# Kernel tuning notes

Measured on AMD Instinct MI355X. Metric: run time of the kernel, lower is better.

The kernel has to match this reference:

```python
import jax, jax.numpy as jnp
import numpy as np
from jax import lax

D = 256      # key/query dim
D_F = 256    # diff feature channels
C_TOK = 1    # leading context tokens in query_vit
EPS = 1e-6


def conv2d(x, w, b, pad):
    out = lax.conv_general_dilated(x, w, (1, 1), [(pad, pad), (pad, pad)],
                                   dimension_numbers=('NCHW', 'OIHW', 'NCHW'))
    return out + b[None, :, None, None]


def gn1(x, g, b):
    # GroupNorm with 1 group: normalize over (C,H,W) per sample
    mu = jnp.mean(x, axis=(1, 2, 3), keepdims=True)
    var = jnp.var(x, axis=(1, 2, 3), keepdims=True)
    xn = (x - mu) * lax.rsqrt(var + EPS)
    return xn * g[None, :, None, None] + b[None, :, None, None]


def resize_bilinear_ac(x, Ho, Wo):
    # F.interpolate(mode='bilinear', align_corners=True)
    B, C, H, W = x.shape
    ys = jnp.linspace(0.0, H - 1.0, Ho)
    xs = jnp.linspace(0.0, W - 1.0, Wo)
    y0 = jnp.floor(ys).astype(jnp.int32)
    y1 = jnp.minimum(y0 + 1, H - 1)
    wy = (ys - y0)[None, None, :, None]
    x0 = jnp.floor(xs).astype(jnp.int32)
    x1 = jnp.minimum(x0 + 1, W - 1)
    wx = (xs - x0)[None, None, None, :]
    r = x[:, :, y0, :] * (1.0 - wy) + x[:, :, y1, :] * wy
    return r[:, :, :, x0] * (1.0 - wx) + r[:, :, :, x1] * wx


def setup_inputs() -> dict:
    key = jax.random.key(0)
    ks = jax.random.split(key, 12)
    B, Hd, Wd, Ht, Wt = 8, 64, 64, 32, 32

    def kaiming(k, shape, fan_in):
        return jax.random.normal(k, shape, jnp.float32) * np.sqrt(2.0 / fan_in)

    return {
        'query_vit': jax.random.normal(ks[0], (B, C_TOK + Ht * Wt, D), jnp.float32),
        'feat_diff_cat': jax.random.normal(ks[1], (B, 5 * D_F, Hd, Wd), jnp.float32),
        'rb_w1': kaiming(ks[2], (D_F, 5 * D_F, 3, 3), 5 * D_F * 9), 'rb_b1': jnp.zeros((D_F,), jnp.float32),
        'rb_w2': kaiming(ks[3], (D_F, D_F, 3, 3), D_F * 9), 'rb_b2': jnp.zeros((D_F,), jnp.float32),
        'rb_ws': kaiming(ks[4], (D_F, 5 * D_F, 1, 1), 5 * D_F), 'rb_bs': jnp.zeros((D_F,), jnp.float32),
        'ln_g': jnp.ones((D_F,), jnp.float32), 'ln_b': jnp.zeros((D_F,), jnp.float32),
        'key_w': kaiming(ks[5], (D, D_F, 1, 1), D_F), 'key_b': jnp.zeros((D,), jnp.float32),
        'val_w': kaiming(ks[6], (D_F, D_F, 1, 1), D_F), 'val_b': jnp.zeros((D_F,), jnp.float32),
        'dh0_w': kaiming(ks[7], (D_F, D_F, 3, 3), D_F * 9), 'dh0_b': jnp.zeros((D_F,), jnp.float32),
        'dh1_w': kaiming(ks[8], (D_F, D_F, 3, 3), D_F * 9), 'dh1_b': jnp.zeros((D_F,), jnp.float32),
    }


def reference(query_vit, feat_diff_cat, rb_w1, rb_b1, rb_w2, rb_b2, rb_ws, rb_bs,
              ln_g, ln_b, key_w, key_b, val_w, val_b, dh0_w, dh0_b, dh1_w, dh1_b):
    B, _, h_diff, w_diff = feat_diff_cat.shape
    N = query_vit.shape[1] - C_TOK
    h_trm = w_trm = int(N ** 0.5)

    # ResBlock_ysh(D_f*5 -> D_f): conv3x3 + relu + conv3x3, 1x1-projected residual
    h = jax.nn.relu(conv2d(feat_diff_cat, rb_w1, rb_b1, 1))
    h = conv2d(h, rb_w2, rb_b2, 1)
    feat_diff = jax.nn.relu(h + conv2d(feat_diff_cat, rb_ws, rb_bs, 0))

    fln = gn1(feat_diff, ln_g, ln_b)
    key_diff = conv2d(fln, key_w, key_b, 0).reshape(B, D, -1)          # (B, D, HW)
    value_diff = conv2d(fln, val_w, val_b, 0).reshape(B, D_F, -1)      # (B, Df, HW)
    value_diff = jnp.transpose(value_diff, (0, 2, 1))                  # (B, HW, Df)

    # cross attention: (B, C+N, D) @ (B, D, HW) -> softmax -> @ (B, HW, Df)
    scores = jnp.einsum('bnd,bdm->bnm', query_vit, key_diff) * (D ** -0.5)
    attn = jax.nn.softmax(scores, axis=-1)
    out_cross = jnp.einsum('bnm,bmf->bnf', attn, value_diff)           # (B, C+N, Df)

    out_cross_c = out_cross[:, :C_TOK, :]
    out_p = jnp.transpose(out_cross[:, C_TOK:, :], (0, 2, 1)).reshape(B, D_F, h_trm, w_trm)
    out_p = jax.nn.relu(conv2d(out_p, dh0_w, dh0_b, 1))
    out_p = resize_bilinear_ac(out_p, h_diff, w_diff)
    out_p = out_p + feat_diff                                          # DropPath(0) = identity
    out_p = jax.nn.relu(conv2d(gn1(out_p, ln_g, ln_b), dh1_w, dh1_b, 1)) + out_p
    return out_cross_c, out_p
```

## Files before the change

kernel.cpp:

```cpp
#include <hip/hip_runtime.h>
#include <cstdint>
#include <cstddef>

typedef __attribute__((ext_vector_type(4))) float     f32x4;
typedef __attribute__((ext_vector_type(8))) __bf16    bf16x8;
typedef __attribute__((ext_vector_type(8))) short     short8;
typedef __attribute__((ext_vector_type(4))) unsigned short u16x4;
typedef unsigned short u16;

__device__ __forceinline__ float b2f(u16 u) {
  unsigned x = ((unsigned)u) << 16;
  float f;
  __builtin_memcpy(&f, &x, 4);
  return f;
}
__device__ __forceinline__ u16 f2b(float f) {
  unsigned u;
  __builtin_memcpy(&u, &f, 4);
  return (u16)((u + 0x7FFFu + ((u >> 16) & 1u)) >> 16);
}

struct GP {
  const u16*  A;
  const u16*  B;
  const float* bias;
  const void* aux;
  void*       C;
  float*      out0;
  long long   aBS, bBS, cBS, auxBS;
  int Ktot, Mrows, ldc;
  int cin, logW, wpad, poff;
  float scale;
};

#define GLDS16(g, l)                                                        \
  __builtin_amdgcn_global_load_lds(                                         \
      (const void __attribute__((address_space(1)))*)(g),                   \
      (void __attribute__((address_space(3)))*)(l), 16, 0, 0)

struct G256 {
  const u16* A;
  const u16* B;
  float* P;
  long long aBS;
  int Ktot, cin, logW, wpad, poff;
};

__global__ __launch_bounds__(512, 2) void k_gemm256(G256 gp) {
  const int tid = threadIdx.x;
  const int l = tid & 63, w = tid >> 6;
  const int lr = l & 15, lc = l >> 4;
  const int mt = blockIdx.x, sp = blockIdx.y, b = blockIdx.z;
  const int m0 = mt << 8;
  const int wm = w >> 2, wn = w & 3;

  __shared__ __align__(16) u16 sm[2][32768];
  u16* smb = &sm[0][0];

  f32x4 acc[8][4];
#pragma unroll
  for (int i = 0; i < 8; ++i)
#pragma unroll
    for (int j = 0; j < 4; ++j) acc[i][j] = (f32x4){0.f, 0.f, 0.f, 0.f};

  const u16* Ab = gp.A + (size_t)b * gp.aBS;
  const int slot = l & 3;
  const u16* aS[2];
  const u16* bS[2];
#pragma unroll
  for (int j = 0; j < 2; ++j) {
    const int r = j * 128 + w * 16 + (l >> 2);
    const int p = m0 + r;
    const int y = p >> gp.logW, x = p & ((1 << gp.logW) - 1);
    const int sw = (slot ^ ((r >> 1) & 3)) << 3;
    aS[j] = Ab + (size_t)((y + gp.poff) * gp.wpad + (x + gp.poff)) * gp.cin + sw;
    bS[j] = gp.B + (size_t)r * gp.Ktot + sw;
  }
  auto dstA = [&](int buf, int ks, int j) -> u16* {
    return smb + buf * 32768 + ks * 8192 + (j * 128 + w * 16) * 32 + l * 8;
  };
  auto dstB = [&](int buf, int ks, int j) -> u16* {
    return smb + buf * 32768 + 16384 + ks * 8192 + (j * 128 + w * 16) * 32 + l * 8;
  };

  const int Thalf = (gp.Ktot >> 6) >> 1;
  const int kt0 = sp * Thalf;
  int off = kt0 << 6;
  int tap = off / gp.cin;
  int kcS = off - tap * gp.cin;
  int dxS = tap % 3;
  int tapS = (tap / 3) * gp.wpad + dxS;
  int ktS = kt0;

  auto adv = [&](int& kA, int& kB) {
    kB = ktS << 6;
    kA = tapS * gp.cin + kcS;
    kcS += 64;
    if (kcS == gp.cin) {
      kcS = 0; ++dxS; ++tapS;
      if (dxS == 3) { dxS = 0; tapS += gp.wpad - 3; }
    }
    ++ktS;
  };

  {
    int kA, kB;
    adv(kA, kB);
    GLDS16(aS[0] + kA, dstA(0, 0, 0));
    GLDS16(aS[1] + kA, dstA(0, 0, 1));
    GLDS16(bS[0] + kB, dstB(0, 0, 0));
    GLDS16(bS[1] + kB, dstB(0, 0, 1));
    GLDS16(aS[0] + kA + 32, dstA(0, 1, 0));
    GLDS16(aS[1] + kA + 32, dstA(0, 1, 1));
    GLDS16(bS[0] + kB + 32, dstB(0, 1, 0));
    GLDS16(bS[1] + kB + 32, dstB(0, 1, 1));
  }
  asm volatile("s_waitcnt vmcnt(4)" ::: "memory");
  __builtin_amdgcn_s_barrier();

  const int NT = Thalf;
  for (int t = 0; t < NT; ++t) {
    const int buf = t & 1;
    const char* base = (const char*)smb + buf * 65536;
    const bool pf = (t + 1 < NT);
    int kA = 0, kB = 0;
    if (pf) adv(kA, kB);

    bf16x8 av[4], bv[4];

#pragma unroll
    for (int mi = 0; mi < 4; ++mi) {
      const int row = wm * 128 + mi * 16 + lr;
      av[mi] = *(const bf16x8*)(base + row * 64 + ((lc ^ ((row >> 1) & 3)) << 4));
    }
#pragma unroll
    for (int ni = 0; ni < 4; ++ni) {
      const int row = wn * 64 + ni * 16 + lr;
      bv[ni] = *(const bf16x8*)(base + 32768 + row * 64 +
                                ((lc ^ ((row >> 1) & 3)) << 4));
    }
    if (pf) {
      GLDS16(aS[0] + kA, dstA(buf ^ 1, 0, 0));
      GLDS16(aS[1] + kA, dstA(buf ^ 1, 0, 1));
    }
    __builtin_amdgcn_s_barrier();
    asm volatile("s_waitcnt lgkmcnt(0)" ::: "memory");
    __builtin_amdgcn_sched_barrier(0);
    __builtin_amdgcn_s_setprio(1);
#pragma unroll
    for (int mi = 0; mi < 4; ++mi)
#pragma unroll
      for (int ni = 0; ni < 4; ++ni)
        acc[mi][ni] = __builtin_amdgcn_mfma_f32_16x16x32_bf16(
            av[mi], bv[ni], acc[mi][ni], 0, 0, 0);
    __builtin_amdgcn_s_setprio(0);
    __builtin_amdgcn_sched_barrier(0);
    __builtin_amdgcn_s_barrier();

#pragma unroll
    for (int mi = 0; mi < 4; ++mi) {
      const int row = wm * 128 + (4 + mi) * 16 + lr;
      av[mi] = *(const bf16x8*)(base + row * 64 + ((lc ^ ((row >> 1) & 3)) << 4));
    }
    if (pf) {
      GLDS16(bS[0] + kB, dstB(buf ^ 1, 0, 0));
      GLDS16(bS[1] + kB, dstB(buf ^ 1, 0, 1));
    }
    __builtin_amdgcn_s_barrier();
    asm volatile("s_waitcnt lgkmcnt(0)" ::: "memory");
    __builtin_amdgcn_sched_barrier(0);
    __builtin_amdgcn_s_setprio(1);
#pragma unroll
    for (int mi = 0; mi < 4; ++mi)
#pragma unroll
      for (int ni = 0; ni < 4; ++ni)
        acc[4 + mi][ni] = __builtin_amdgcn_mfma_f32_16x16x32_bf16(
            av[mi], bv[ni], acc[4 + mi][ni], 0, 0, 0);
    __builtin_amdgcn_s_setprio(0);
    __builtin_amdgcn_sched_barrier(0);
    if (pf)
      asm volatile("s_waitcnt vmcnt(4)" ::: "memory");
    else
      asm volatile("s_waitcnt vmcnt(0)" ::: "memory");
    __builtin_amdgcn_s_barrier();

#pragma unroll
    for (int mi = 0; mi < 4; ++mi) {
      const int row = wm * 128 + mi * 16 + lr;
      av[mi] = *(const bf16x8*)(base + 16384 + row * 64 +
                                ((lc ^ ((row >> 1) & 3)) << 4));
    }
#pragma unroll
    for (int ni = 0; ni < 4; ++ni) {
      const int row = wn * 64 + ni * 16 + lr;
      bv[ni] = *(const bf16x8*)(base + 49152 + row * 64 +
                                ((lc ^ ((row >> 1) & 3)) << 4));
    }
    if (pf) {
      GLDS16(aS[0] + kA + 32, dstA(buf ^ 1, 1, 0));
      GLDS16(aS[1] + kA + 32, dstA(buf ^ 1, 1, 1));
    }
    __builtin_amdgcn_s_barrier();
    asm volatile("s_waitcnt lgkmcnt(0)" ::: "memory");
    __builtin_amdgcn_sched_barrier(0);
    __builtin_amdgcn_s_setprio(1);
#pragma unroll
    for (int mi = 0; mi < 4; ++mi)
#pragma unroll
      for (int ni = 0; ni < 4; ++ni)
        acc[mi][ni] = __builtin_amdgcn_mfma_f32_16x16x32_bf16(
            av[mi], bv[ni], acc[mi][ni], 0, 0, 0);
    __builtin_amdgcn_s_setprio(0);
    __builtin_amdgcn_sched_barrier(0);
    __builtin_amdgcn_s_barrier();

#pragma unroll
    for (int mi = 0; mi < 4; ++mi) {
      const int row = wm * 128 + (4 + mi) * 16 + lr;
      av[mi] = *(const bf16x8*)(base + 16384 + row * 64 +
                                ((lc ^ ((row >> 1) & 3)) << 4));
    }
    if (pf) {
      GLDS16(bS[0] + kB + 32, dstB(buf ^ 1, 1, 0));
      GLDS16(bS[1] + kB + 32, dstB(buf ^ 1, 1, 1));
    }
    __builtin_amdgcn_s_barrier();
    asm volatile("s_waitcnt lgkmcnt(0)" ::: "memory");
    __builtin_amdgcn_sched_barrier(0);
    __builtin_amdgcn_s_setprio(1);
#pragma unroll
    for (int mi = 0; mi < 4; ++mi)
#pragma unroll
      for (int ni = 0; ni < 4; ++ni)
        acc[4 + mi][ni] = __builtin_amdgcn_mfma_f32_16x16x32_bf16(
            av[mi], bv[ni], acc[4 + mi][ni], 0, 0, 0);
    __builtin_amdgcn_s_setprio(0);
    __builtin_amdgcn_sched_barrier(0);
    if (pf) {
      asm volatile("s_waitcnt vmcnt(4)" ::: "memory");
      __builtin_amdgcn_s_barrier();
    }
  }

  float* P = gp.P + ((size_t)sp * 128 + b * 16 + mt) * 65536;
#pragma unroll
  for (int mi = 0; mi < 8; ++mi)
#pragma unroll
    for (int ni = 0; ni < 4; ++ni) {
      const int ncol = wn * 64 + ni * 16 + lr;
      const int mloc = wm * 128 + mi * 16 + lc * 4;
#pragma unroll
      for (int r = 0; r < 4; ++r)
        P[(size_t)(mloc + r) * 256 + ncol] = acc[mi][ni][r];
    }
}

__global__ __launch_bounds__(256) void k_reduceH1(const float* __restrict__ P,
                                                  const float* __restrict__ bias,
                                                  u16* __restrict__ o) {
  const int i4 = blockIdx.x * 256 + threadIdx.x;
  const int flat = i4 << 2;
  const int n0 = flat & 255;
  const int mloc = (flat >> 8) & 255;
  const int gm = flat >> 16;
  const f32x4 a = *(const f32x4*)(P + (size_t)gm * 65536 + mloc * 256 + n0);
  const f32x4 c = *(const f32x4*)(P + (size_t)(128 + gm) * 65536 + mloc * 256 + n0);
  const f32x4 bb = *(const f32x4*)(bias + n0);
  const int batch = gm >> 4;
  const int mg = (gm & 15) * 256 + mloc;
  const int y = mg >> 6, x = mg & 63;
  u16x4 r;
#pragma unroll
  for (int k = 0; k < 4; ++k) r[k] = f2b(fmaxf(a[k] + c[k] + bb[k], 0.f));
  *(u16x4*)(o + ((size_t)batch * 4356 + (size_t)(y + 1) * 66 + x + 1) * 256 + n0) = r;
}

template <int AMODE, int CW, bool RELU>
__global__ __launch_bounds__(512, 2) void k_gemm8(GP gp) {
  const int tid = threadIdx.x;
  const int l = tid & 63, w = tid >> 6;
  const int b = blockIdx.z;
  const int m0 = blockIdx.x * 128;
  const int wm = w >> 2, wn = w & 3;

  __shared__ __align__(16) u16 sm[3][24576];

  f32x4 acc[4][4];
#pragma unroll
  for (int i = 0; i < 4; ++i)
#pragma unroll
    for (int j = 0; j < 4; ++j) acc[i][j] = (f32x4){0.f, 0.f, 0.f, 0.f};

  const u16* Ab = gp.A + (size_t)b * gp.aBS;
  const u16* Bb = gp.B + (size_t)b * gp.bBS;
  const int scoff = (((tid & 7) ^ ((tid >> 3) & 7)) << 3);

  const u16* aP[2];
  const u16* bP[4];
#pragma unroll
  for (int i = 0; i < 2; ++i) {
    const int p = m0 + i * 64 + (tid >> 3);
    if (AMODE == 0) {
      const int pc = p < gp.Mrows ? p : gp.Mrows - 1;
      aP[i] = Ab + (size_t)pc * gp.Ktot + scoff;
    } else {
      const int y = p >> gp.logW, x = p & ((1 << gp.logW) - 1);
      aP[i] = Ab + (size_t)((y + gp.poff) * gp.wpad + (x + gp.poff)) * gp.cin +
              scoff;
    }
  }
#pragma unroll
  for (int i = 0; i < 4; ++i)
    bP[i] = Bb + (size_t)(i * 64 + (tid >> 3)) * gp.Ktot + scoff;

  const int NT = gp.Ktot >> 6;
  int kcS = 0, tapS = 0, dxS = 0, ktS = 0;

  auto adv = [&](int& kA, int& kB) {
    kB = ktS << 6;
    if (AMODE == 0) {
      kA = ktS << 6;
    } else {
      kA = tapS * gp.cin + kcS;
      kcS += 64;
      if (kcS == gp.cin) {
        kcS = 0; ++dxS; ++tapS;
        if (dxS == 3) { dxS = 0; tapS += gp.wpad - 3; }
      }
    }
    ++ktS;
  };

#pragma unroll
  for (int pt = 0; pt < 2; ++pt) {
    int kA, kB;
    adv(kA, kB);
    u16* sA = &sm[pt][0] + (w << 9);
    u16* sB = &sm[pt][8192] + (w << 9);
    GLDS16(aP[0] + kA, sA);
    GLDS16(aP[1] + kA, sA + 4096);
    GLDS16(bP[0] + kB, sB);
    GLDS16(bP[1] + kB, sB + 4096);
    GLDS16(bP[2] + kB, sB + 8192);
    GLDS16(bP[3] + kB, sB + 12288);
  }
  asm volatile("s_waitcnt vmcnt(6)" ::: "memory");
  __builtin_amdgcn_s_barrier();

  const int lr = l & 15, lc = l >> 4;
  int bufC = 0, bufS = 2;

  for (int t = 0; t < NT; ++t) {
    const u16* sAc = &sm[bufC][0];
    const u16* sBc = &sm[bufC][8192];
    const bool sOK = (t + 2 < NT);
    int kAs = 0, kBs = 0;
    if (sOK) adv(kAs, kBs);
    u16* sAs = &sm[bufS][0] + (w << 9);
    u16* sBs = &sm[bufS][8192] + (w << 9);

    bf16x8 bv[4][2];
    {
      bf16x8 av[2][2];
#pragma unroll
      for (int mi = 0; mi < 2; ++mi) {
        const int row = wm * 64 + mi * 16 + lr;
#pragma unroll
        for (int ks = 0; ks < 2; ++ks) {
          const int cc = ks * 4 + lc;
          av[mi][ks] =
              *(const bf16x8*)(sAc + row * 64 + ((cc ^ (row & 7)) << 3));
        }
      }
#pragma unroll
      for (int ni = 0; ni < 4; ++ni) {
        const int row = wn * 64 + ni * 16 + lr;
#pragma unroll
        for (int ks = 0; ks < 2; ++ks) {
          const int cc = ks * 4 + lc;
          bv[ni][ks] =
              *(const bf16x8*)(sBc + row * 64 + ((cc ^ (row & 7)) << 3));
        }
      }
      if (sOK) {
        GLDS16(aP[0] + kAs, sAs);
        GLDS16(aP[1] + kAs, sAs + 4096);
        GLDS16(bP[0] + kBs, sBs);
      }
      __builtin_amdgcn_s_barrier();
      asm volatile("s_waitcnt lgkmcnt(0)" ::: "memory");
      __builtin_amdgcn_sched_barrier(0);
      __builtin_amdgcn_s_setprio(1);
#pragma unroll
      for (int ks = 0; ks < 2; ++ks)
#pragma unroll
        for (int mi = 0; mi < 2; ++mi)
#pragma unroll
          for (int ni = 0; ni < 4; ++ni)
            acc[mi][ni] = __builtin_amdgcn_mfma_f32_16x16x32_bf16(
                av[mi][ks], bv[ni][ks], acc[mi][ni], 0, 0, 0);
      __builtin_amdgcn_sched_barrier(0);
      __builtin_amdgcn_s_setprio(0);
    }
    __builtin_amdgcn_s_barrier();
    {
      bf16x8 av[2][2];
#pragma unroll
      for (int mi = 0; mi < 2; ++mi) {
        const int row = wm * 64 + (mi + 2) * 16 + lr;
#pragma unroll
        for (int ks = 0; ks < 2; ++ks) {
          const int cc = ks * 4 + lc;
          av[mi][ks] =
              *(const bf16x8*)(sAc + row * 64 + ((cc ^ (row & 7)) << 3));
        }
      }
      if (sOK) {
        GLDS16(bP[1] + kBs, sBs + 4096);
        GLDS16(bP[2] + kBs, sBs + 8192);
        GLDS16(bP[3] + kBs, sBs + 12288);
      }
      __builtin_amdgcn_s_barrier();
      asm volatile("s_waitcnt lgkmcnt(0)" ::: "memory");
      __builtin_amdgcn_sched_barrier(0);
      __builtin_amdgcn_s_setprio(1);
#pragma unroll
      for (int ks = 0; ks < 2; ++ks)
#pragma unroll
        for (int mi = 0; mi < 2; ++mi)
#pragma unroll
          for (int ni = 0; ni < 4; ++ni)
            acc[mi + 2][ni] = __builtin_amdgcn_mfma_f32_16x16x32_bf16(
                av[mi][ks], bv[ni][ks], acc[mi + 2][ni], 0, 0, 0);
      __builtin_amdgcn_sched_barrier(0);
      __builtin_amdgcn_s_setprio(0);
    }
    if (t + 1 < NT) {
      if (t + 2 < NT)
        asm volatile("s_waitcnt vmcnt(6)" ::: "memory");
      else
        asm volatile("s_waitcnt vmcnt(0)" ::: "memory");
      __builtin_amdgcn_s_barrier();
    }
    bufC = bufC == 2 ? 0 : bufC + 1;
    bufS = bufS == 2 ? 0 : bufS + 1;
  }

#pragma unroll
  for (int mi = 0; mi < 4; ++mi) {
#pragma unroll
    for (int ni = 0; ni < 4; ++ni) {
      const int ncol = wn * 64 + ni * 16 + lr;
      const int mbase = m0 + wm * 64 + mi * 16 + lc * 4;
      const float bv_ = gp.bias ? gp.bias[ncol] : 0.f;
      if constexpr (CW == 0) {
#pragma unroll
        for (int r = 0; r < 4; ++r) {
          float v = acc[mi][ni][r] + bv_;
          if (RELU) v = fmaxf(v, 0.f);
          ((u16*)gp.C)[(size_t)b * gp.cBS + (size_t)(mbase + r) * 256 + ncol] =
              f2b(v);
        }
      } else if constexpr (CW == 1) {
#pragma unroll
        for (int r = 0; r < 4; ++r) {
          float v = acc[mi][ni][r] + bv_;
          if (RELU) v = fmaxf(v, 0.f);
          const int mrow = mbase + r;
          const int y = mrow >> 6, x = mrow & 63;
          ((u16*)gp.C)[(size_t)b * gp.cBS +
                       (size_t)((y + 1) * 66 + x + 1) * 256 + ncol] = f2b(v);
        }
      } else if constexpr (CW == 2) {
#pragma unroll
        for (int r = 0; r < 4; ++r) {
          const int mrow = mbase + r;
          const float s =
              b2f(((const u16*)gp.aux)[(size_t)b * gp.auxBS +
                                       (size_t)mrow * 256 + ncol]);
          float v = acc[mi][ni][r] + bv_ + s;
          v = fmaxf(v, 0.f);
          ((float*)gp.C)[(size_t)b * gp.cBS + (size_t)mrow * 256 + ncol] = v;
        }
      } else if constexpr (CW == 6) {
        float* Cf =
            (float*)gp.C + (size_t)b * gp.cBS + (size_t)ncol * 4096 + mbase;
        const float* mid = (const float*)gp.aux + (size_t)b * gp.auxBS;
        f32x4 o;
#pragma unroll
        for (int r = 0; r < 4; ++r) {
          float v = acc[mi][ni][r] + bv_;
          v = fmaxf(v, 0.f);
          o[r] = v + mid[(size_t)(mbase + r) * 256 + ncol];
        }
        *(f32x4*)Cf = o;
      }
    }
  }
}

template <int AMODE, int CW, bool RELU>
__global__ __launch_bounds__(256, 2) void k_gemm(GP gp) {
  const int tid = threadIdx.x;
  const int l = tid & 63, w = tid >> 6;
  const int b = blockIdx.z;
  const int m0 = blockIdx.x * 128, n0 = blockIdx.y * 128;
  const int wm = w >> 1, wn = w & 1;

  __shared__ __align__(16) u16 smA[128 * 64];
  __shared__ __align__(16) u16 smB[128 * 64];

  f32x4 acc[4][4];
#pragma unroll
  for (int i = 0; i < 4; ++i)
#pragma unroll
    for (int j = 0; j < 4; ++j) acc[i][j] = (f32x4){0.f, 0.f, 0.f, 0.f};

  const u16* Ab = gp.A + (size_t)b * gp.aBS;
  const u16* Bb = gp.B + (size_t)b * gp.bBS;

  const int scoff = (((l & 7) ^ (l >> 3)) << 3);

  const u16* aRow[4];
  const u16* bRow[4];
  u16* ldsA[4];
  u16* ldsB[4];
#pragma unroll
  for (int i = 0; i < 4; ++i) {
    const int r = w * 32 + i * 8 + (l >> 3);
    bRow[i] = Bb + (size_t)(n0 + r) * gp.Ktot + scoff;
    const int p = m0 + r;
    if (AMODE == 0) {
      const int pc = p < gp.Mrows ? p : gp.Mrows - 1;
      aRow[i] = Ab + (size_t)pc * gp.Ktot + scoff;
    } else {
      const int y = p >> gp.logW, x = p & ((1 << gp.logW) - 1);
      const int icoord = (y + gp.poff) * gp.wpad + (x + gp.poff);
      aRow[i] = Ab + (size_t)icoord * gp.cin + scoff;
    }
    ldsA[i] = smA + (w * 32 + i * 8) * 64;
    ldsB[i] = smB + (w * 32 + i * 8) * 64;
  }

  const int ktiles = gp.Ktot >> 6;
  int tap_off = 0, dx = 0, kc = 0;

  for (int kt = 0; kt < ktiles; ++kt) {
    int koffA;
    if (AMODE == 0)
      koffA = kt << 6;
    else
      koffA = tap_off * gp.cin + kc;
    const int koffB = kt << 6;
#pragma unroll
    for (int i = 0; i < 4; ++i) GLDS16(aRow[i] + koffA, ldsA[i]);
#pragma unroll
    for (int i = 0; i < 4; ++i) GLDS16(bRow[i] + koffB, ldsB[i]);

    if (AMODE == 1) {
      kc += 64;
      if (kc == gp.cin) {
        kc = 0;
        ++dx;
        ++tap_off;
        if (dx == 3) { dx = 0; tap_off += gp.wpad - 3; }
      }
    }

    __syncthreads();
#pragma unroll
    for (int ks = 0; ks < 2; ++ks) {
      bf16x8 av[4], bv[4];
      const int cc = (ks << 2) + (l >> 4);
#pragma unroll
      for (int mi = 0; mi < 4; ++mi) {
        const int row = wm * 64 + mi * 16 + (l & 15);
        av[mi] = *(const bf16x8*)((const char*)smA + (row << 7) +
                                  ((cc ^ (row & 7)) << 4));
      }
#pragma unroll
      for (int ni = 0; ni < 4; ++ni) {
        const int row = wn * 64 + ni * 16 + (l & 15);
        bv[ni] = *(const bf16x8*)((const char*)smB + (row << 7) +
                                  ((cc ^ (row & 7)) << 4));
      }
#pragma unroll
      for (int mi = 0; mi < 4; ++mi)
#pragma unroll
        for (int ni = 0; ni < 4; ++ni)
          acc[mi][ni] = __builtin_amdgcn_mfma_f32_16x16x32_bf16(
              av[mi], bv[ni], acc[mi][ni], 0, 0, 0);
    }
    __syncthreads();
  }

#pragma unroll
  for (int mi = 0; mi < 4; ++mi) {
#pragma unroll
    for (int ni = 0; ni < 4; ++ni) {
      const int ncol = n0 + wn * 64 + ni * 16 + (l & 15);
      const int mbase = m0 + wm * 64 + mi * 16 + ((l >> 4) << 2);
      const float bv_ = gp.bias ? gp.bias[ncol] : 0.f;

      if constexpr (CW == 3) {
        u16* Cu = (u16*)gp.C + (size_t)b * gp.cBS + (size_t)ncol * 4096 + mbase;
        u16x4 pk;
#pragma unroll
        for (int r = 0; r < 4; ++r) pk[r] = f2b(acc[mi][ni][r] + bv_);
        *(u16x4*)Cu = pk;
      } else if constexpr (CW == 7) {
        u16* base = (u16*)gp.C;
        if (ncol < 256) {
#pragma unroll
          for (int r = 0; r < 4; ++r)
            base[(size_t)b * 1048576 + (size_t)(mbase + r) * 256 + ncol] =
                f2b(acc[mi][ni][r] + bv_);
        } else {
          u16x4 pk;
#pragma unroll
          for (int r = 0; r < 4; ++r) pk[r] = f2b(acc[mi][ni][r] + bv_);
          *(u16x4*)(base + 8388608 + (size_t)b * 1048576 +
                    (size_t)(ncol - 256) * 4096 + mbase) = pk;
        }
      } else {
#pragma unroll
        for (int reg = 0; reg < 4; ++reg) {
          const int mrow = mbase + reg;
          if (mrow >= gp.Mrows) continue;
          float v = acc[mi][ni][reg] * gp.scale + bv_;
          if (RELU) v = v > 0.f ? v : 0.f;
          if constexpr (CW == 0) {
            ((u16*)gp.C)[(size_t)b * gp.cBS + (size_t)mrow * gp.ldc + ncol] =
                f2b(v);
          } else if constexpr (CW == 4) {
            if (mrow == 0) {
              gp.out0[(size_t)b * 256 + ncol] = v;
            } else {
              const int p = mrow - 1, y = p >> 5, x = p & 31;
              ((u16*)gp.C)[(size_t)b * gp.cBS +
                           (size_t)((y + 1) * 34 + (x + 1)) * 256 + ncol] =
                  f2b(v);
            }
          } else if constexpr (CW == 5) {
            ((float*)gp.C)[(size_t)b * gp.cBS + (size_t)mrow * 256 + ncol] = v;
          }
        }
      }
    }
  }
}


__global__ __launch_bounds__(256) void k_prep_x(const float* __restrict__ x,
                                                u16* __restrict__ o) {
  __shared__ float t[32][65];
  const int b = blockIdx.z, c0 = blockIdx.y << 5, y = blockIdx.x;
  const float* src = x + ((size_t)b * 1280 + c0) * 4096 + (size_t)y * 64;
#pragma unroll
  for (int i = 0; i < 8; ++i) {
    const int idx = threadIdx.x + (i << 8);
    const int c = idx >> 6, xx = idx & 63;
    t[c][xx] = src[(size_t)c * 4096 + xx];
  }
  __syncthreads();
  u16* dst = o + ((size_t)b * 4356 + (size_t)(y + 1) * 66 + 1) * 1280 + c0;
#pragma unroll
  for (int i = 0; i < 8; ++i) {
    const int idx = threadIdx.x + (i << 8);
    const int xx = idx >> 5, c = idx & 31;
    dst[(size_t)xx * 1280 + c] = f2b(t[c][xx]);
  }
}

__global__ __launch_bounds__(256) void k_zero_border(u16* __restrict__ p,
                                                     int P, int C) {
  const int per_img = (4 * P - 4) * C;
  const int total = 8 * per_img;
  for (int idx = blockIdx.x * 256 + threadIdx.x; idx < total;
       idx += gridDim.x * 256) {
    const int b = idx / per_img;
    const int r = idx % per_img;
    const int pix = r / C, c = r % C;
    int y, x;
    const int Pm = P - 1;
    if (pix < P) { y = 0; x = pix; }
    else if (pix < 2 * P) { y = Pm; x = pix - P; }
    else if (pix < 3 * P - 2) { y = pix - 2 * P + 1; x = 0; }
    else { y = pix - (3 * P - 2) + 1; x = Pm; }
    p[((size_t)b * P * P + (size_t)y * P + x) * C + c] = 0;
  }
}

__global__ __launch_bounds__(256) void k_prep_w3(const float* __restrict__ w,
                                                 u16* __restrict__ o, int cin,
                                                 int n) {
  for (int i = blockIdx.x * 256 + threadIdx.x; i < n; i += gridDim.x * 256) {
    const int ci = i % cin;
    const int r = i / cin;
    const int t = r % 9;
    const int co = r / 9;
    o[i] = f2b(w[((size_t)co * cin + ci) * 9 + t]);
  }
}

__global__ __launch_bounds__(256) void k_f2b(const float* __restrict__ x,
                                             u16* __restrict__ o, int n) {
  for (int i = blockIdx.x * 256 + threadIdx.x; i < n; i += gridDim.x * 256)
    o[i] = f2b(x[i]);
}

__global__ __launch_bounds__(256) void k_gn_stats(const float* __restrict__ x,
                                                  float* __restrict__ st) {
  const int b = blockIdx.y;
  const f32x4* xb = (const f32x4*)(x + (size_t)b * 1048576);
  float s = 0.f, s2 = 0.f;
  for (int i = blockIdx.x * 256 + threadIdx.x; i < 262144;
       i += gridDim.x * 256) {
    const f32x4 v = xb[i];
    s += v[0] + v[1] + v[2] + v[3];
    s2 += v[0] * v[0] + v[1] * v[1] + v[2] * v[2] + v[3] * v[3];
  }
#pragma unroll
  for (int o = 32; o; o >>= 1) {
    s += __shfl_down(s, o);
    s2 += __shfl_down(s2, o);
  }
  __shared__ float ls[4], ls2[4];
  const int w = threadIdx.x >> 6;
  if ((threadIdx.x & 63) == 0) { ls[w] = s; ls2[w] = s2; }
  __syncthreads();
  if (threadIdx.x == 0) {
    atomicAdd(&st[b * 2], ls[0] + ls[1] + ls[2] + ls[3]);
    atomicAdd(&st[b * 2 + 1], ls2[0] + ls2[1] + ls2[2] + ls2[3]);
  }
}

template <bool PAD>
__global__ __launch_bounds__(256) void k_gn_norm(const float* __restrict__ x,
                                                 const float* __restrict__ st,
                                                 const float* __restrict__ g,
                                                 const float* __restrict__ bb,
                                                 u16* __restrict__ o) {
  const int b = blockIdx.y;
  const float mu = st[b * 2] * (1.f / 1048576.f);
  const float var = st[b * 2 + 1] * (1.f / 1048576.f) - mu * mu;
  const float rs = rsqrtf(var + 1e-6f);
  const int i4 = blockIdx.x * 256 + threadIdx.x;
  const f32x4 v = ((const f32x4*)(x + (size_t)b * 1048576))[i4];
  const int flat = i4 << 2;
  const int c = flat & 255;
  const int p = flat >> 8;
  const f32x4 gv = *(const f32x4*)(g + c);
  const f32x4 bv = *(const f32x4*)(bb + c);
  u16x4 r;
#pragma unroll
  for (int k = 0; k < 4; ++k) r[k] = f2b((v[k] - mu) * rs * gv[k] + bv[k]);
  size_t oidx;
  if (PAD) {
    const int y = p >> 6, xx = p & 63;
    oidx = ((size_t)b * 4356 + (size_t)(y + 1) * 66 + xx + 1) * 256 + c;
  } else {
    oidx = ((size_t)b * 4096 + p) * 256 + c;
  }
  *(u16x4*)(o + oidx) = r;
}

__global__ __launch_bounds__(256) void k_softmax(u16* __restrict__ s) {
  const size_t row = blockIdx.x;
  u16* p = s + row * 4096;
  const int t = threadIdx.x;
  const short8 r0 = ((const short8*)p)[t];
  const short8 r1 = ((const short8*)p)[t + 256];
  float v[16];
#pragma unroll
  for (int i = 0; i < 8; ++i) {
    v[i] = b2f((u16)r0[i]);
    v[8 + i] = b2f((u16)r1[i]);
  }
  float m = v[0];
#pragma unroll
  for (int i = 1; i < 16; ++i) m = fmaxf(m, v[i]);
#pragma unroll
  for (int o = 32; o; o >>= 1) m = fmaxf(m, __shfl_xor(m, o));
  __shared__ float lm[4], lsum[4];
  const int w = t >> 6;
  if ((t & 63) == 0) lm[w] = m;
  __syncthreads();
  m = fmaxf(fmaxf(lm[0], lm[1]), fmaxf(lm[2], lm[3]));
  float sum = 0.f;
#pragma unroll
  for (int i = 0; i < 16; ++i) {
    v[i] = __expf(v[i] - m);
    sum += v[i];
  }
#pragma unroll
  for (int o = 32; o; o >>= 1) sum += __shfl_xor(sum, o);
  if ((t & 63) == 0) lsum[w] = sum;
  __syncthreads();
  sum = lsum[0] + lsum[1] + lsum[2] + lsum[3];
  const float inv = 1.f / sum;
  short8 o0, o1;
#pragma unroll
  for (int i = 0; i < 8; ++i) {
    o0[i] = (short)f2b(v[i] * inv);
    o1[i] = (short)f2b(v[8 + i] * inv);
  }
  ((short8*)p)[t] = o0;
  ((short8*)p)[t + 256] = o1;
}

__global__ __launch_bounds__(256) void k_resize_add(const float* __restrict__ d0,
                                                    const float* __restrict__ F,
                                                    float* __restrict__ mid) {
  const int i4 = blockIdx.x * 256 + threadIdx.x;
  const int flat = i4 << 2;
  const int c = flat & 255;
  const int p = (flat >> 8) & 4095;
  const int b = flat >> 20;
  const int y = p >> 6, x = p & 63;
  const float fy = y * (31.f / 63.f);
  const int y0 = (int)fy;
  const float wy = fy - y0;
  const int y1 = y0 + 1 > 31 ? 31 : y0 + 1;
  const float fx = x * (31.f / 63.f);
  const int x0 = (int)fx;
  const float wx = fx - x0;
  const int x1 = x0 + 1 > 31 ? 31 : x0 + 1;
  const float* db = d0 + (size_t)b * 262144;
  const f32x4 a = *(const f32x4*)(db + ((size_t)(y0 * 32 + x0) << 8) + c);
  const f32x4 bq = *(const f32x4*)(db + ((size_t)(y0 * 32 + x1) << 8) + c);
  const f32x4 cq = *(const f32x4*)(db + ((size_t)(y1 * 32 + x0) << 8) + c);
  const f32x4 dq = *(const f32x4*)(db + ((size_t)(y1 * 32 + x1) << 8) + c);
  f32x4 r = (a * (1.f - wx) + bq * wx) * (1.f - wy) +
            (cq * (1.f - wx) + dq * wx) * wy;
  r += *(const f32x4*)(F + (size_t)flat);
  *(f32x4*)(mid + (size_t)flat) = r;
}


extern "C" void kernel_launch(void* const* d_in, const int* in_sizes, int n_in,
                              void* d_out, int out_size, void* d_ws,
                              size_t ws_size, hipStream_t stream) {
  (void)in_sizes; (void)n_in; (void)out_size;

  const float* q   = (const float*)d_in[0];
  const float* xdc = (const float*)d_in[1];
  const float* w1  = (const float*)d_in[2];
  const float* b1  = (const float*)d_in[3];
  const float* w2  = (const float*)d_in[4];
  const float* b2  = (const float*)d_in[5];
  const float* wsc = (const float*)d_in[6];
  const float* bsc = (const float*)d_in[7];
  const float* lng = (const float*)d_in[8];
  const float* lnb = (const float*)d_in[9];
  const float* wk  = (const float*)d_in[10];
  const float* bk  = (const float*)d_in[11];
  const float* wv  = (const float*)d_in[12];
  const float* bv  = (const float*)d_in[13];
  const float* wd0 = (const float*)d_in[14];
  const float* bd0 = (const float*)d_in[15];
  const float* wd1 = (const float*)d_in[16];
  const float* bd1 = (const float*)d_in[17];

  char* ws = (char*)d_ws;
  size_t cur = 0;
  auto alloc = [&](size_t sz) {
    char* p = ws + cur;
    cur += sz;
    return p;
  };
  u16* XPAD = (u16*)alloc(89194496);
  u16* W1R  = (u16*)alloc(5898240);
  u16* W2R  = (u16*)alloc(1179648);
  u16* WSR  = (u16*)alloc(655360);
  u16* WKV  = (u16*)alloc(262144);
  float* BKV = (float*)alloc(2048);
  u16* WD0R = (u16*)alloc(1179648);
  u16* WD1R = (u16*)alloc(1179648);
  u16* SB   = (u16*)alloc(16777216);
  u16* H1   = (u16*)alloc(17842176);
  float* F  = (float*)alloc(33554432);
  u16* FLN  = (u16*)alloc(16777216);
  u16* KT   = (u16*)alloc(16777216);
  u16* V    = (u16*)alloc(16777216);
  u16* QB   = (u16*)alloc(4198400);
  u16* OCP  = (u16*)alloc(4734976);
  float* D0O = (float*)alloc(8388608);
  float* MID = (float*)alloc(33554432);
  u16* G2   = (u16*)alloc(17842176);
  float* ST = (float*)alloc(256);
  u16* SCORES = XPAD;
  float* PART = (float*)FLN;
  (void)V;

  if (ws_size < cur) return;

  float* out0 = (float*)d_out;
  float* out1 = (float*)d_out + 2048;

  hipMemsetAsync(ST, 0, 256, stream);
  hipMemcpyAsync(BKV, bk, 1024, hipMemcpyDeviceToDevice, stream);
  hipMemcpyAsync(BKV + 256, bv, 1024, hipMemcpyDeviceToDevice, stream);

  k_zero_border<<<2048, 256, 0, stream>>>(XPAD, 66, 1280);
  k_zero_border<<<1024, 256, 0, stream>>>(H1, 66, 256);
  k_zero_border<<<1024, 256, 0, stream>>>(G2, 66, 256);

  k_prep_x<<<dim3(64, 40, 8), 256, 0, stream>>>(xdc, XPAD);
  k_prep_w3<<<2048, 256, 0, stream>>>(w1, W1R, 1280, 2949120);
  k_prep_w3<<<1024, 256, 0, stream>>>(w2, W2R, 256, 589824);
  k_prep_w3<<<1024, 256, 0, stream>>>(wd0, WD0R, 256, 589824);
  k_prep_w3<<<1024, 256, 0, stream>>>(wd1, WD1R, 256, 589824);
  k_f2b<<<512, 256, 0, stream>>>(wsc, WSR, 327680);
  k_f2b<<<128, 256, 0, stream>>>(wk, WKV, 65536);
  k_f2b<<<128, 256, 0, stream>>>(wv, WKV + 65536, 65536);

  const dim3 g8(32, 1, 8);
  {
    GP g{};
    g.A = XPAD; g.B = WSR; g.bias = bsc; g.C = SB;
    g.aBS = 5575680; g.bBS = 0; g.cBS = 1048576;
    g.Ktot = 1280; g.Mrows = 4096; g.ldc = 256;
    g.cin = 1280; g.logW = 6; g.wpad = 66; g.poff = 1; g.scale = 1.f;
    k_gemm8<1, 0, false><<<g8, 512, 0, stream>>>(g);
  }
  {
    G256 g{};
    g.A = XPAD; g.B = W1R; g.P = PART;
    g.aBS = 5575680; g.Ktot = 11520;
    g.cin = 1280; g.logW = 6; g.wpad = 66; g.poff = 0;
    k_gemm256<<<dim3(16, 2, 8), 512, 0, stream>>>(g);
    k_reduceH1<<<8192, 256, 0, stream>>>(PART, b1, H1);
  }
  k_f2b<<<2048, 256, 0, stream>>>(q, QB, 2099200);
  k_zero_border<<<512, 256, 0, stream>>>(OCP, 34, 256);

  {
    GP g{};
    g.A = H1; g.B = W2R; g.bias = b2; g.C = F; g.aux = SB;
    g.aBS = 1115136; g.bBS = 0; g.cBS = 1048576; g.auxBS = 1048576;
    g.Ktot = 2304; g.Mrows = 4096; g.ldc = 256;
    g.cin = 256; g.logW = 6; g.wpad = 66; g.poff = 0; g.scale = 1.f;
    k_gemm8<1, 2, false><<<g8, 512, 0, stream>>>(g);
  }
  k_gn_stats<<<dim3(64, 8), 256, 0, stream>>>(F, ST);
  k_gn_norm<false><<<dim3(1024, 8), 256, 0, stream>>>(F, ST, lng, lnb, FLN);
  {
    GP g{};
    g.A = FLN; g.B = WKV; g.bias = BKV; g.C = KT;
    g.aBS = 1048576; g.bBS = 0; g.cBS = 0;
    g.Ktot = 256; g.Mrows = 4096; g.ldc = 256; g.scale = 1.f;
    k_gemm<0, 7, false><<<dim3(32, 4, 8), 256, 0, stream>>>(g);
  }
  {
    GP g{};
    g.A = QB; g.B = KT; g.bias = nullptr; g.C = SCORES;
    g.aBS = 262400; g.bBS = 1048576; g.cBS = 4198400;
    g.Ktot = 256; g.Mrows = 1025; g.ldc = 4096; g.scale = 0.0625f;
    k_gemm<0, 0, false><<<dim3(9, 32, 8), 256, 0, stream>>>(g);
  }
  k_softmax<<<8200, 256, 0, stream>>>(SCORES);
  {
    GP g{};
    g.A = SCORES; g.B = V; g.bias = nullptr; g.C = OCP; g.out0 = out0;
    g.aBS = 4198400; g.bBS = 1048576; g.cBS = 295936;
    g.Ktot = 4096; g.Mrows = 1025; g.ldc = 256; g.scale = 1.f;
    k_gemm<0, 4, false><<<dim3(9, 2, 8), 256, 0, stream>>>(g);
  }
  {
    GP g{};
    g.A = OCP; g.B = WD0R; g.bias = bd0; g.C = D0O;
    g.aBS = 295936; g.bBS = 0; g.cBS = 262144;
    g.Ktot = 2304; g.Mrows = 1024; g.ldc = 256;
    g.cin = 256; g.logW = 5; g.wpad = 34; g.poff = 0; g.scale = 1.f;
    k_gemm<1, 5, true><<<dim3(8, 2, 8), 256, 0, stream>>>(g);
  }
  k_resize_add<<<8192, 256, 0, stream>>>(D0O, F, MID);
  k_gn_stats<<<dim3(64, 8), 256, 0, stream>>>(MID, ST + 16);
  k_gn_norm<true><<<dim3(1024, 8), 256, 0, stream>>>(MID, ST + 16, lng, lnb, G2);
  {
    GP g{};
    g.A = G2; g.B = WD1R; g.bias = bd1; g.C = out1; g.aux = MID;
    g.aBS = 1115136; g.bBS = 0; g.cBS = 1048576; g.auxBS = 1048576;
    g.Ktot = 2304; g.Mrows = 4096; g.ldc = 256;
    g.cin = 256; g.logW = 6; g.wpad = 66; g.poff = 0; g.scale = 1.f;
    k_gemm8<1, 6, false><<<g8, 512, 0, stream>>>(g);
  }
}
```

Baseline: 724.2 us.

## Simplify GEMM main loops to plain double-buffering with one barrier per step

After: 730.7 us. No clear change (+0.9%).

```diff
diff --git a/kernel.cpp b/kernel.cpp
--- a/kernel.cpp
+++ b/kernel.cpp
@@ -115,7 +115,7 @@
     GLDS16(bS[0] + kB + 32, dstB(0, 1, 0));
     GLDS16(bS[1] + kB + 32, dstB(0, 1, 1));
   }
-  asm volatile("s_waitcnt vmcnt(4)" ::: "memory");
+  asm volatile("s_waitcnt vmcnt(0)" ::: "memory");
   __builtin_amdgcn_s_barrier();
 
   const int NT = Thalf;
@@ -123,123 +123,51 @@
     const int buf = t & 1;
     const char* base = (const char*)smb + buf * 65536;
     const bool pf = (t + 1 < NT);
-    int kA = 0, kB = 0;
-    if (pf) adv(kA, kB);
-
-    bf16x8 av[4], bv[4];
-
-#pragma unroll
-    for (int mi = 0; mi < 4; ++mi) {
-      const int row = wm * 128 + mi * 16 + lr;
-      av[mi] = *(const bf16x8*)(base + row * 64 + ((lc ^ ((row >> 1) & 3)) << 4));
-    }
+    if (pf) {
+      int kA, kB;
+      adv(kA, kB);
+      GLDS16(aS[0] + kA, dstA(buf ^ 1, 0, 0));
+      GLDS16(aS[1] + kA, dstA(buf ^ 1, 0, 1));
+      GLDS16(bS[0] + kB, dstB(buf ^ 1, 0, 0));
+      GLDS16(bS[1] + kB, dstB(buf ^ 1, 0, 1));
+      GLDS16(aS[0] + kA + 32, dstA(buf ^ 1, 1, 0));
+      GLDS16(aS[1] + kA + 32, dstA(buf ^ 1, 1, 1));
+      GLDS16(bS[0] + kB + 32, dstB(buf ^ 1, 1, 0));
+      GLDS16(bS[1] + kB + 32, dstB(buf ^ 1, 1, 1));
+    }
+    bf16x8 bv0[4], bv1[4];
 #pragma unroll
     for (int ni = 0; ni < 4; ++ni) {
       const int row = wn * 64 + ni * 16 + lr;
-      bv[ni] = *(const bf16x8*)(base + 32768 + row * 64 +
-                                ((lc ^ ((row >> 1) & 3)) << 4));
-    }
-    if (pf) {
-      GLDS16(aS[0] + kA, dstA(buf ^ 1, 0, 0));
-      GLDS16(aS[1] + kA, dstA(buf ^ 1, 0, 1));
-    }
+      const int sw = (lc ^ ((row >> 1) & 3)) << 4;
+      bv0[ni] = *(const bf16x8*)(base + 32768 + row * 64 + sw);
+      bv1[ni] = *(const bf16x8*)(base + 49152 + row * 64 + sw);
+    }
+#pragma unroll
+    for (int mq = 0; mq < 2; ++mq) {
+      bf16x8 a0[4], a1[4];
+#pragma unroll
+      for (int mi = 0; mi < 4; ++mi) {
+        const int row = wm * 128 + (mq * 4 + mi) * 16 + lr;
+        const int sw = (lc ^ ((row >> 1) & 3)) << 4;
+        a0[mi] = *(const bf16x8*)(base + row * 64 + sw);
+        a1[mi] = *(const bf16x8*)(base + 16384 + row * 64 + sw);
+      }
+#pragma unroll
+      for (int mi = 0; mi < 4; ++mi)
+#pragma unroll
+        for (int ni = 0; ni < 4; ++ni)
+          acc[mq * 4 + mi][ni] = __builtin_amdgcn_mfma_f32_16x16x32_bf16(
+              a0[mi], bv0[ni], acc[mq * 4 + mi][ni], 0, 0, 0);
+#pragma unroll
+      for (int mi = 0; mi < 4; ++mi)
+#pragma unroll
+        for (int ni = 0; ni < 4; ++ni)
+          acc[mq * 4 + mi][ni] = __builtin_amdgcn_mfma_f32_16x16x32_bf16(
+              a1[mi], bv1[ni], acc[mq * 4 + mi][ni], 0, 0, 0);
+    }
+    asm volatile("s_waitcnt vmcnt(0)" ::: "memory");
     __builtin_amdgcn_s_barrier();
-    asm volatile("s_waitcnt lgkmcnt(0)" ::: "memory");
-    __builtin_amdgcn_sched_barrier(0);
-    __builtin_amdgcn_s_setprio(1);
-#pragma unroll
-    for (int mi = 0; mi < 4; ++mi)
-#pragma unroll
-      for (int ni = 0; ni < 4; ++ni)
-        acc[mi][ni] = __builtin_amdgcn_mfma_f32_16x16x32_bf16(
-            av[mi], bv[ni], acc[mi][ni], 0, 0, 0);
-    __builtin_amdgcn_s_setprio(0);
-    __builtin_amdgcn_sched_barrier(0);
-    __builtin_amdgcn_s_barrier();
-
-#pragma unroll
-    for (int mi = 0; mi < 4; ++mi) {
-      const int row = wm * 128 + (4 + mi) * 16 + lr;
-      av[mi] = *(const bf16x8*)(base + row * 64 + ((lc ^ ((row >> 1) & 3)) << 4));
-    }
-    if (pf) {
-      GLDS16(bS[0] + kB, dstB(buf ^ 1, 0, 0));
-      GLDS16(bS[1] + kB, dstB(buf ^ 1, 0, 1));
-    }
-    __builtin_amdgcn_s_barrier();
-    asm volatile("s_waitcnt lgkmcnt(0)" ::: "memory");
-    __builtin_amdgcn_sched_barrier(0);
-    __builtin_amdgcn_s_setprio(1);
-#pragma unroll
-    for (int mi = 0; mi < 4; ++mi)
-#pragma unroll
-      for (int ni = 0; ni < 4; ++ni)
-        acc[4 + mi][ni] = __builtin_amdgcn_mfma_f32_16x16x32_bf16(
-            av[mi], bv[ni], acc[4 + mi][ni], 0, 0, 0);
-    __builtin_amdgcn_s_setprio(0);
-    __builtin_amdgcn_sched_barrier(0);
-    if (pf)
-      asm volatile("s_waitcnt vmcnt(4)" ::: "memory");
-    else
-      asm volatile("s_waitcnt vmcnt(0)" ::: "memory");
-    __builtin_amdgcn_s_barrier();
-
-#pragma unroll
-    for (int mi = 0; mi < 4; ++mi) {
-      const int row = wm * 128 + mi * 16 + lr;
-      av[mi] = *(const bf16x8*)(base + 16384 + row * 64 +
-                                ((lc ^ ((row >> 1) & 3)) << 4));
-    }
-#pragma unroll
-    for (int ni = 0; ni < 4; ++ni) {
-      const int row = wn * 64 + ni * 16 + lr;
-      bv[ni] = *(const bf16x8*)(base + 49152 + row * 64 +
-                                ((lc ^ ((row >> 1) & 3)) << 4));
-    }
-    if (pf) {
-      GLDS16(aS[0] + kA + 32, dstA(buf ^ 1, 1, 0));
-      GLDS16(aS[1] + kA + 32, dstA(buf ^ 1, 1, 1));
-    }
-    __builtin_amdgcn_s_barrier();
-    asm volatile("s_waitcnt lgkmcnt(0)" ::: "memory");
-    __builtin_amdgcn_sched_barrier(0);
-    __builtin_amdgcn_s_setprio(1);
-#pragma unroll
-    for (int mi = 0; mi < 4; ++mi)
-#pragma unroll
-      for (int ni = 0; ni < 4; ++ni)
-        acc[mi][ni] = __builtin_amdgcn_mfma_f32_16x16x32_bf16(
-            av[mi], bv[ni], acc[mi][ni], 0, 0, 0);
-    __builtin_amdgcn_s_setprio(0);
-    __builtin_amdgcn_sched_barrier(0);
-    __builtin_amdgcn_s_barrier();
-
-#pragma unroll
-    for (int mi = 0; mi < 4; ++mi) {
-      const int row = wm * 128 + (4 + mi) * 16 + lr;
-      av[mi] = *(const bf16x8*)(base + 16384 + row * 64 +
-                                ((lc ^ ((row >> 1) & 3)) << 4));
-    }
-    if (pf) {
-      GLDS16(bS[0] + kB + 32, dstB(buf ^ 1, 1, 0));
-      GLDS16(bS[1] + kB + 32, dstB(buf ^ 1, 1, 1));
-    }
-    __builtin_amdgcn_s_barrier();
-    asm volatile("s_waitcnt lgkmcnt(0)" ::: "memory");
-    __builtin_amdgcn_sched_barrier(0);
-    __builtin_amdgcn_s_setprio(1);
-#pragma unroll
-    for (int mi = 0; mi < 4; ++mi)
-#pragma unroll
-      for (int ni = 0; ni < 4; ++ni)
-        acc[4 + mi][ni] = __builtin_amdgcn_mfma_f32_16x16x32_bf16(
-            av[mi], bv[ni], acc[4 + mi][ni], 0, 0, 0);
-    __builtin_amdgcn_s_setprio(0);
-    __builtin_amdgcn_sched_barrier(0);
-    if (pf) {
-      asm volatile("s_waitcnt vmcnt(4)" ::: "memory");
-      __builtin_amdgcn_s_barrier();
-    }
   }
 
   float* P = gp.P + ((size_t)sp * 128 + b * 16 + mt) * 65536;
@@ -282,8 +210,9 @@
   const int b = blockIdx.z;
   const int m0 = blockIdx.x * 128;
   const int wm = w >> 2, wn = w & 3;
-
-  __shared__ __align__(16) u16 sm[3][24576];
+  const int lr = l & 15, lc = l >> 4;
+
+  __shared__ __align__(16) u16 sm[2][24576];
 
   f32x4 acc[4][4];
 #pragma unroll
@@ -331,12 +260,11 @@
     ++ktS;
   };
 
-#pragma unroll
-  for (int pt = 0; pt < 2; ++pt) {
+  {
     int kA, kB;
     adv(kA, kB);
-    u16* sA = &sm[pt][0] + (w << 9);
-    u16* sB = &sm[pt][8192] + (w << 9);
+    u16* sA = &sm[0][0] + (w << 9);
+    u16* sB = &sm[0][8192] + (w << 9);
     GLDS16(aP[0] + kA, sA);
     GLDS16(aP[1] + kA, sA + 4096);
     GLDS16(bP[0] + kB, sB);
@@ -344,106 +272,53 @@
     GLDS16(bP[2] + kB, sB + 8192);
     GLDS16(bP[3] + kB, sB + 12288);
   }
-  asm volatile("s_waitcnt vmcnt(6)" ::: "memory");
+  asm volatile("s_waitcnt vmcnt(0)" ::: "memory");
   __builtin_amdgcn_s_barrier();
 
-  const int lr = l & 15, lc = l >> 4;
-  int bufC = 0, bufS = 2;
-
   for (int t = 0; t < NT; ++t) {
-    const u16* sAc = &sm[bufC][0];
-    const u16* sBc = &sm[bufC][8192];
-    const bool sOK = (t + 2 < NT);
-    int kAs = 0, kBs = 0;
-    if (sOK) adv(kAs, kBs);
-    u16* sAs = &sm[bufS][0] + (w << 9);
-    u16* sBs = &sm[bufS][8192] + (w << 9);
-
-    bf16x8 bv[4][2];
-    {
-      bf16x8 av[2][2];
-#pragma unroll
-      for (int mi = 0; mi < 2; ++mi) {
-        const int row = wm * 64 + mi * 16 + lr;
-#pragma unroll
-        for (int ks = 0; ks < 2; ++ks) {
-          const int cc = ks * 4 + lc;
-          av[mi][ks] =
-              *(const bf16x8*)(sAc + row * 64 + ((cc ^ (row & 7)) << 3));
-        }
-      }
-#pragma unroll
-      for (int ni = 0; ni < 4; ++ni) {
-        const int row = wn * 64 + ni * 16 + lr;
-#pragma unroll
-        for (int ks = 0; ks < 2; ++ks) {
-          const int cc = ks * 4 + lc;
-          bv[ni][ks] =
-              *(const bf16x8*)(sBc + row * 64 + ((cc ^ (row & 7)) << 3));
-        }
-      }
-      if (sOK) {
-        GLDS16(aP[0] + kAs, sAs);
-        GLDS16(aP[1] + kAs, sAs + 4096);
-        GLDS16(bP[0] + kBs, sBs);
-      }
-      __builtin_amdgcn_s_barrier();
-      asm volatile("s_waitcnt lgkmcnt(0)" ::: "memory");
-      __builtin_amdgcn_sched_barrier(0);
-      __builtin_amdgcn_s_setprio(1);
-#pragma unroll
-      for (int ks = 0; ks < 2; ++ks)
-#pragma unroll
-        for (int mi = 0; mi < 2; ++mi)
-#pragma unroll
-          for (int ni = 0; ni < 4; ++ni)
-            acc[mi][ni] = __builtin_amdgcn_mfma_f32_16x16x32_bf16(
-                av[mi][ks], bv[ni][ks], acc[mi][ni], 0, 0, 0);
-      __builtin_amdgcn_sched_barrier(0);
-      __builtin_amdgcn_s_setprio(0);
-    }
+    const int buf = t & 1;
+    const u16* sAc = &sm[buf][0];
+    const u16* sBc = &sm[buf][8192];
+    const bool pf = (t + 1 < NT);
+    if (pf) {
+      int kA, kB;
+      adv(kA, kB);
+      u16* sA = &sm[buf ^ 1][0] + (w << 9);
+      u16* sB = &sm[buf ^ 1][8192] + (w << 9);
+      GLDS16(aP[0] + kA, sA);
+      GLDS16(aP[1] + kA, sA + 4096);
+      GLDS16(bP[0] + kB, sB);
+      GLDS16(bP[1] + kB, sB + 4096);
+      GLDS16(bP[2] + kB, sB + 8192);
+      GLDS16(bP[3] + kB, sB + 12288);
+    }
+    bf16x8 av0[4], av1[4], bv0[4], bv1[4];
+#pragma unroll
+    for (int mi = 0; mi < 4; ++mi) {
+      const int row = wm * 64 + mi * 16 + lr;
+      av0[mi] = *(const bf16x8*)(sAc + row * 64 + (((0 + lc) ^ (row & 7)) << 3));
+      av1[mi] = *(const bf16x8*)(sAc + row * 64 + (((4 + lc) ^ (row & 7)) << 3));
+    }
+#pragma unroll
+    for (int ni = 0; ni < 4; ++ni) {
+      const int row = wn * 64 + ni * 16 + lr;
+      bv0[ni] = *(const bf16x8*)(sBc + row * 64 + (((0 + lc) ^ (row & 7)) << 3));
+      bv1[ni] = *(const bf16x8*)(sBc + row * 64 + (((4 + lc) ^ (row & 7)) << 3));
+    }
+#pragma unroll
+    for (int mi = 0; mi < 4; ++mi)
+#pragma unroll
+      for (int ni = 0; ni < 4; ++ni)
+        acc[mi][ni] = __builtin_amdgcn_mfma_f32_16x16x32_bf16(
+            av0[mi], bv0[ni], acc[mi][ni], 0, 0, 0);
+#pragma unroll
+    for (int mi = 0; mi < 4; ++mi)
+#pragma unroll
+      for (int ni = 0; ni < 4; ++ni)
+        acc[mi][ni] = __builtin_amdgcn_mfma_f32_16x16x32_bf16(
+            av1[mi], bv1[ni], acc[mi][ni], 0, 0, 0);
+    asm volatile("s_waitcnt vmcnt(0)" ::: "memory");
     __builtin_amdgcn_s_barrier();
-    {
-      bf16x8 av[2][2];
-#pragma unroll
-      for (int mi = 0; mi < 2; ++mi) {
-        const int row = wm * 64 + (mi + 2) * 16 + lr;
-#pragma unroll
-        for (int ks = 0; ks < 2; ++ks) {
-          const int cc = ks * 4 + lc;
-          av[mi][ks] =
-              *(const bf16x8*)(sAc + row * 64 + ((cc ^ (row & 7)) << 3));
-        }
-      }
-      if (sOK) {
-        GLDS16(bP[1] + kBs, sBs + 4096);
-        GLDS16(bP[2] + kBs, sBs + 8192);
-        GLDS16(bP[3] + kBs, sBs + 12288);
-      }
-      __builtin_amdgcn_s_barrier();
-      asm volatile("s_waitcnt lgkmcnt(0)" ::: "memory");
-      __builtin_amdgcn_sched_barrier(0);
-      __builtin_amdgcn_s_setprio(1);
-#pragma unroll
-      for (int ks = 0; ks < 2; ++ks)
-#pragma unroll
-        for (int mi = 0; mi < 2; ++mi)
-#pragma unroll
-          for (int ni = 0; ni < 4; ++ni)
-            acc[mi + 2][ni] = __builtin_amdgcn_mfma_f32_16x16x32_bf16(
-                av[mi][ks], bv[ni][ks], acc[mi + 2][ni], 0, 0, 0);
-      __builtin_amdgcn_sched_barrier(0);
-      __builtin_amdgcn_s_setprio(0);
-    }
-    if (t + 1 < NT) {
-      if (t + 2 < NT)
-        asm volatile("s_waitcnt vmcnt(6)" ::: "memory");
-      else
-        asm volatile("s_waitcnt vmcnt(0)" ::: "memory");
-      __builtin_amdgcn_s_barrier();
-    }
-    bufC = bufC == 2 ? 0 : bufC + 1;
-    bufS = bufS == 2 ? 0 : bufS + 1;
   }
 
 #pragma unroll
```
